# Optimization experiments

Hardware: AMD Instinct MI355X
Metric: run time of the kernel (lower is better)

Reference implementation:

```python
import jax, jax.numpy as jnp
import numpy as np

ROPE_BASE = 10000.0

def _rope_cos_sin(T, d, dtype):
    inv_freq = 1.0 / (ROPE_BASE ** (jnp.arange(0, d, 2, dtype=jnp.float32) / d))
    t = jnp.arange(T, dtype=jnp.float32)
    freqs = t[:, None] * inv_freq[None, :]           # [T, d/2]
    emb = jnp.concatenate([freqs, freqs], axis=-1)   # [T, d]
    return jnp.cos(emb).astype(dtype), jnp.sin(emb).astype(dtype)

def _rotate_half(x):
    x1, x2 = jnp.split(x, 2, axis=-1)
    return jnp.concatenate([-x2, x1], axis=-1)

def setup_inputs() -> dict:
    key = jax.random.key(0)
    k1, k2, k3, k4 = jax.random.split(key, 4)
    B, T, C, H = 4, 4096, 1024, 64
    x = jax.random.normal(k1, (B, T, C), dtype=jnp.float32)
    s = 1.0 / np.sqrt(C)
    Wq = jax.random.normal(k2, (H, C), dtype=jnp.float32) * s
    Wk = jax.random.normal(k3, (H, C), dtype=jnp.float32) * s
    Wv = jax.random.normal(k4, (H, C), dtype=jnp.float32) * s
    return {"x": x, "Wq": Wq, "Wk": Wk, "Wv": Wv}

def reference(x, Wq, Wk, Wv):
    B, T, C = x.shape
    H = Wq.shape[0]
    q = jnp.einsum('btc,hc->bth', x, Wq)
    k = jnp.einsum('btc,hc->bth', x, Wk)
    v = jnp.einsum('btc,hc->bth', x, Wv)
    cos, sin = _rope_cos_sin(T, H, x.dtype)
    q = q * cos + _rotate_half(q) * sin
    k = k * cos + _rotate_half(k) * sin
    # NOTE: original scales by dim_model**-0.5 (C), not head_size
    wei = jnp.einsum('bth,bsh->bts', q, k) * (C ** -0.5)
    causal = jnp.tril(jnp.ones((T, T), dtype=bool))
    wei = jnp.where(causal, wei, -jnp.inf)
    wei = jax.nn.softmax(wei, axis=-1)
    # dropout p=0.0 (identity)
    out = jnp.einsum('bts,bsh->bth', wei, v)
    return out
```

## Files before the change

### kernel.cpp

```cpp
#include <hip/hip_runtime.h>
#include <hip/hip_bf16.h>
#include <math.h>

typedef __attribute__((ext_vector_type(8))) __bf16 bf16x8;
typedef __attribute__((ext_vector_type(4))) float f32x4;
typedef __attribute__((ext_vector_type(16))) float f32x16;
typedef __attribute__((ext_vector_type(4))) float float4_t;
typedef __attribute__((ext_vector_type(4))) unsigned int uint4_t;

#define NB 4
#define TSEQ 4096
#define CD 1024
#define HD 64
#define NCH 16
#define CHT 4

static __device__ __forceinline__ unsigned short f2bf(float f) {
    union { float f; unsigned u; } v; v.f = f;
    unsigned r = v.u + 0x7fffu + ((v.u >> 16) & 1u);
    return (unsigned short)(r >> 16);
}
static __device__ __forceinline__ float bf2f(unsigned short u) {
    union { unsigned int i; float f; } v; v.i = ((unsigned int)u) << 16;
    return v.f;
}
static __device__ __forceinline__ unsigned int pk2(float a, float b) {
    union { __bf16 h[2]; unsigned int u; } x;
    x.h[0] = (__bf16)a; x.h[1] = (__bf16)b;
    return x.u;
}

__global__ __launch_bounds__(256) void wcvt_kernel(const float* __restrict__ wq,
                                                   const float* __restrict__ wk,
                                                   const float* __restrict__ wv,
                                                   unsigned short* __restrict__ wb) {
    int i = blockIdx.x * 256 + threadIdx.x;
    int j = i >> 10;
    int col = i & 1023;
    int jb = j >> 4, off = j & 15;
    int sub = ((jb & 1) << 5) | ((jb & 2) << 3);
    int srcrow = (jb < 8) ? (sub + off) : ((jb - 8) * 16 + off);
    const float* src = (jb < 4) ? wq : ((jb < 8) ? wk : wv);
    wb[i] = f2bf(src[srcrow * 1024 + col]);
}

__global__ __launch_bounds__(256) void qkv_kernel(const float* __restrict__ x,
                                                  const unsigned short* __restrict__ wb,
                                                  unsigned short* __restrict__ qo,
                                                  unsigned short* __restrict__ ko,
                                                  unsigned short* __restrict__ vt) {
    __shared__ unsigned short xs[64][72];
    __shared__ unsigned short ws[64][72];
    const int tid = threadIdx.x;
    const int wave = tid >> 6, lane = tid & 63;
    const int lr = lane & 15;
    const int lk = (lane >> 4) << 3;
    const int rowg = (lane >> 4) << 2;
    const int row0 = blockIdx.x * 64;
    const int cbi = blockIdx.y;
    const int cb = cbi * 64;

    f32x4 acc[4];
#pragma unroll
    for (int i = 0; i < 4; ++i) acc[i] = (f32x4){0.f, 0.f, 0.f, 0.f};

    const int sr = tid >> 2;
    const int sc = (tid & 3) << 4;

    for (int k0 = 0; k0 < CD; k0 += 64) {
        __syncthreads();
        {
            const float4_t* s4 =
                reinterpret_cast<const float4_t*>(x + (size_t)(row0 + sr) * CD + k0 + sc);
            alignas(16) unsigned short tmp[16];
#pragma unroll
            for (int j = 0; j < 4; ++j) {
                float4_t f = s4[j];
#pragma unroll
                for (int e = 0; e < 4; ++e) tmp[j * 4 + e] = f2bf(f[e]);
            }
            *reinterpret_cast<uint4_t*>(&xs[sr][sc]) = *reinterpret_cast<const uint4_t*>(&tmp[0]);
            *reinterpret_cast<uint4_t*>(&xs[sr][sc + 8]) = *reinterpret_cast<const uint4_t*>(&tmp[8]);
        }
        {
            const uint4_t* wsrc =
                reinterpret_cast<const uint4_t*>(wb + (size_t)(cb + sr) * CD + k0 + sc);
            *reinterpret_cast<uint4_t*>(&ws[sr][sc]) = wsrc[0];
            *reinterpret_cast<uint4_t*>(&ws[sr][sc + 8]) = wsrc[1];
        }
        __syncthreads();
#pragma unroll
        for (int kk = 0; kk < 2; ++kk) {
            bf16x8 a = *reinterpret_cast<const bf16x8*>(&xs[wave * 16 + lr][kk * 32 + lk]);
#pragma unroll
            for (int c = 0; c < 4; ++c) {
                bf16x8 bfr = *reinterpret_cast<const bf16x8*>(&ws[c * 16 + lr][kk * 32 + lk]);
                acc[c] = __builtin_amdgcn_mfma_f32_16x16x32_bf16(a, bfr, acc[c], 0, 0, 0);
            }
        }
    }

    const int gr0 = row0 + wave * 16 + rowg;
    const int bidx = gr0 >> 12;
    const int tb = gr0 & (TSEQ - 1);
    if (cbi < 2) {
        unsigned short* o = (cbi == 0) ? qo : ko;
        const float sc2 = (cbi == 0) ? 0.045084218764560315f : 1.0f;
        const float l2b = 0.4152410118609215f;
        const float invf0 = exp2f(-(float)lr * l2b);
        const float invf1 = exp2f(-(float)(lr + 16) * l2b);
#pragma unroll
        for (int r = 0; r < 4; ++r) {
            float t = (float)(tb + r);
            float s0, c0, s1, c1;
            sincosf(t * invf0, &s0, &c0);
            sincosf(t * invf1, &s1, &c1);
            size_t ro = (size_t)(gr0 + r) * HD;
            float lo, hi;
            lo = acc[0][r]; hi = acc[1][r];
            o[ro + 0 + lr]  = f2bf((lo * c0 - hi * s0) * sc2);
            o[ro + 32 + lr] = f2bf((hi * c0 + lo * s0) * sc2);
            lo = acc[2][r]; hi = acc[3][r];
            o[ro + 16 + lr] = f2bf((lo * c1 - hi * s1) * sc2);
            o[ro + 48 + lr] = f2bf((hi * c1 + lo * s1) * sc2);
        }
    } else {
#pragma unroll
        for (int r = 0; r < 4; ++r) {
            size_t vbase = (size_t)bidx * HD * TSEQ + (size_t)(tb + r);
            vt[vbase + (size_t)(0 + lr) * TSEQ]  = f2bf(acc[0][r]);
            vt[vbase + (size_t)(16 + lr) * TSEQ] = f2bf(acc[1][r]);
            vt[vbase + (size_t)(32 + lr) * TSEQ] = f2bf(acc[2][r]);
            vt[vbase + (size_t)(48 + lr) * TSEQ] = f2bf(acc[3][r]);
        }
    }
}

__global__ __launch_bounds__(128, 3) void attn_partial(const unsigned short* __restrict__ q,
                                                       const unsigned short* __restrict__ k,
                                                       const unsigned short* __restrict__ vt,
                                                       unsigned short* __restrict__ po,
                                                       float* __restrict__ pm,
                                                       float* __restrict__ pl) {
    const int chunk = blockIdx.x, qt = blockIdx.y, b = blockIdx.z;
    const int kt0 = chunk * CHT;
    if (kt0 > qt) return;
    const int ktend = min(qt, kt0 + CHT - 1);

    __shared__ unsigned short ks[64][72];
    __shared__ unsigned short vs[64][72];
    const int tid = threadIdx.x;
    const int wave = tid >> 6, lane = tid & 63;
    const int l31 = lane & 31;
    const int h = lane >> 5;
    const int h8 = h << 3;
    const int qrow0 = qt * 64 + wave * 32;
    const int qpos = qrow0 + l31;

    const unsigned short* qb_ = q + ((size_t)(b * TSEQ + qpos)) * HD + h8;
    bf16x8 qf[4];
#pragma unroll
    for (int s = 0; s < 4; ++s)
        qf[s] = *reinterpret_cast<const bf16x8*>(qb_ + 16 * s);

    f32x16 oacc[2];
#pragma unroll
    for (int dt = 0; dt < 2; ++dt)
#pragma unroll
        for (int r = 0; r < 16; ++r) oacc[dt][r] = 0.f;
    float mreg = -INFINITY;
    float lsum = 0.f;

    const int srow = tid >> 1;
    const int scol = (tid & 1) << 5;
    const unsigned short* kbase = k + (size_t)b * TSEQ * HD;
    const unsigned short* vbase = vt + (size_t)b * HD * TSEQ;
    uint4_t kr[4], vr[4];
    {
        const int s0l = kt0 * 64;
        const unsigned short* kp = kbase + (size_t)(s0l + srow) * HD + scol;
        const unsigned short* vp = vbase + (size_t)srow * TSEQ + s0l + scol;
#pragma unroll
        for (int j = 0; j < 4; ++j) {
            kr[j] = *reinterpret_cast<const uint4_t*>(kp + 8 * j);
            vr[j] = *reinterpret_cast<const uint4_t*>(vp + 8 * j);
        }
    }

    for (int kt = kt0; kt <= ktend; ++kt) {
        const int s0 = kt * 64;
        __syncthreads();
#pragma unroll
        for (int j = 0; j < 4; ++j) {
            *reinterpret_cast<uint4_t*>(&ks[srow][scol + 8 * j]) = kr[j];
            *reinterpret_cast<uint4_t*>(&vs[srow][scol + 8 * j]) = vr[j];
        }
        __syncthreads();
        if (kt < ktend) {
            const int s0l = s0 + 64;
            const unsigned short* kp = kbase + (size_t)(s0l + srow) * HD + scol;
            const unsigned short* vp = vbase + (size_t)srow * TSEQ + s0l + scol;
#pragma unroll
            for (int j = 0; j < 4; ++j) {
                kr[j] = *reinterpret_cast<const uint4_t*>(kp + 8 * j);
                vr[j] = *reinterpret_cast<const uint4_t*>(vp + 8 * j);
            }
        }

        f32x16 sacc[2];
#pragma unroll
        for (int blk = 0; blk < 2; ++blk)
#pragma unroll
            for (int r = 0; r < 16; ++r) sacc[blk][r] = 0.f;
        __builtin_amdgcn_s_setprio(1);
#pragma unroll
        for (int s = 0; s < 4; ++s) {
            bf16x8 ka = *reinterpret_cast<const bf16x8*>(&ks[l31][16 * s + h8]);
            bf16x8 kb2 = *reinterpret_cast<const bf16x8*>(&ks[32 + l31][16 * s + h8]);
            sacc[0] = __builtin_amdgcn_mfma_f32_32x32x16_bf16(ka, qf[s], sacc[0], 0, 0, 0);
            sacc[1] = __builtin_amdgcn_mfma_f32_32x32x16_bf16(kb2, qf[s], sacc[1], 0, 0, 0);
        }
        __builtin_amdgcn_s_setprio(0);

        if (kt == qt) {
#pragma unroll
            for (int blk = 0; blk < 2; ++blk)
#pragma unroll
                for (int r = 0; r < 16; ++r) {
                    int kvpos = s0 + 32 * blk + (r & 3) + ((r >> 2) << 3) + (h << 2);
                    if (kvpos > qpos) sacc[blk][r] = -INFINITY;
                }
        }

        float tm[8];
#pragma unroll
        for (int r = 0; r < 8; ++r)
            tm[r] = fmaxf(fmaxf(sacc[0][r], sacc[0][r + 8]),
                          fmaxf(sacc[1][r], sacc[1][r + 8]));
#pragma unroll
        for (int r = 0; r < 4; ++r) tm[r] = fmaxf(tm[r], tm[r + 4]);
        float mx = fmaxf(fmaxf(tm[0], tm[1]), fmaxf(tm[2], tm[3]));
        mx = fmaxf(mx, __shfl_xor(mx, 32, 64));

        const bool newmax = !__all(mx <= mreg + 7.0f);
        if (newmax) {
            float mnew = fmaxf(mreg, mx);
            float corr = __builtin_amdgcn_exp2f(mreg - mnew);
            mreg = mnew;
            lsum *= corr;
#pragma unroll
            for (int dt = 0; dt < 2; ++dt)
#pragma unroll
                for (int r = 0; r < 16; ++r) oacc[dt][r] *= corr;
        }

        float pvv[2][16];
#pragma unroll
        for (int blk = 0; blk < 2; ++blk)
#pragma unroll
            for (int r = 0; r < 16; ++r)
                pvv[blk][r] = __builtin_amdgcn_exp2f(sacc[blk][r] - mreg);
        float ts[8];
#pragma unroll
        for (int r = 0; r < 8; ++r)
            ts[r] = (pvv[0][r] + pvv[0][r + 8]) + (pvv[1][r] + pvv[1][r + 8]);
#pragma unroll
        for (int r = 0; r < 4; ++r) ts[r] += ts[r + 4];
        float psum = (ts[0] + ts[1]) + (ts[2] + ts[3]);
        psum += __shfl_xor(psum, 32, 64);
        lsum += psum;

        unsigned int cw[2][4][2];
#pragma unroll
        for (int blk = 0; blk < 2; ++blk)
#pragma unroll
            for (int G = 0; G < 4; ++G) {
                cw[blk][G][0] = pk2(pvv[blk][4 * G], pvv[blk][4 * G + 1]);
                cw[blk][G][1] = pk2(pvv[blk][4 * G + 2], pvv[blk][4 * G + 3]);
            }

        const bool hif = (h == 1);
        __builtin_amdgcn_s_setprio(1);
#pragma unroll
        for (int s = 0; s < 4; ++s) {
            const int blk = s >> 1, base = (s & 1) << 1;
            unsigned int a0 = cw[blk][base][0],     a1 = cw[blk][base][1];
            unsigned int b0 = cw[blk][base + 1][0], b1 = cw[blk][base + 1][1];
            unsigned int s0w = hif ? a0 : b0;
            unsigned int s1w = hif ? a1 : b1;
            unsigned int r0 = __shfl_xor(s0w, 32, 64);
            unsigned int r1 = __shfl_xor(s1w, 32, 64);
            uint4_t pw;
            pw[0] = hif ? r0 : a0;
            pw[1] = hif ? r1 : a1;
            pw[2] = hif ? b0 : r0;
            pw[3] = hif ? b1 : r1;
            bf16x8 pfrag = *reinterpret_cast<const bf16x8*>(&pw);
            bf16x8 v0 = *reinterpret_cast<const bf16x8*>(&vs[l31][16 * s + h8]);
            bf16x8 v1 = *reinterpret_cast<const bf16x8*>(&vs[32 + l31][16 * s + h8]);
            oacc[0] = __builtin_amdgcn_mfma_f32_32x32x16_bf16(v0, pfrag, oacc[0], 0, 0, 0);
            oacc[1] = __builtin_amdgcn_mfma_f32_32x32x16_bf16(v1, pfrag, oacc[1], 0, 0, 0);
        }
        __builtin_amdgcn_s_setprio(0);
    }

    const int slot = (((b << 6) + qt) << 4) + chunk;
    unsigned short* pob = po + (size_t)slot * 4096;
#pragma unroll
    for (int dt = 0; dt < 2; ++dt)
#pragma unroll
        for (int r = 0; r < 16; ++r) {
            int d = 32 * dt + (r & 3) + ((r >> 2) << 3) + (h << 2);
            pob[d * 64 + wave * 32 + l31] = f2bf(oacc[dt][r]);
        }
    if (h == 0) {
        pm[slot * 64 + wave * 32 + l31] = mreg;
        pl[slot * 64 + wave * 32 + l31] = lsum;
    }
}

__global__ __launch_bounds__(256) void attn_combine(const unsigned short* __restrict__ po,
                                                    const float* __restrict__ pm,
                                                    const float* __restrict__ pl,
                                                    float* __restrict__ out) {
    __shared__ float sm[64][68];
    const int bq = blockIdx.x;
    const int qt = bq & 63;
    const int nch = (qt >> 2) + 1;
    const int qi = threadIdx.x & 63;
    const int dg = threadIdx.x >> 6;
    const int sbase = bq << 4;

    float M = -INFINITY;
    for (int c = 0; c < nch; ++c) M = fmaxf(M, pm[(sbase + c) * 64 + qi]);
    float L = 0.f;
    float acc[16];
#pragma unroll
    for (int j = 0; j < 16; ++j) acc[j] = 0.f;
    for (int c = 0; c < nch; ++c) {
        int s = sbase + c;
        float w = exp2f(pm[s * 64 + qi] - M);
        L += w * pl[s * 64 + qi];
        const unsigned short* p = po + (size_t)s * 4096 + qi;
#pragma unroll
        for (int j = 0; j < 16; ++j) acc[j] += w * bf2f(p[(dg * 16 + j) * 64]);
    }
    float inv = 1.f / L;
#pragma unroll
    for (int j = 0; j < 16; ++j) sm[qi][dg * 16 + j] = acc[j] * inv;
    __syncthreads();
    const int row = threadIdx.x >> 2;
    const int cg = (threadIdx.x & 3) << 4;
    float4_t* dst = reinterpret_cast<float4_t*>(out + (size_t)bq * 4096 + row * 64 + cg);
#pragma unroll
    for (int v4 = 0; v4 < 4; ++v4) {
        float4_t f;
#pragma unroll
        for (int e = 0; e < 4; ++e) f[e] = sm[row][cg + v4 * 4 + e];
        dst[v4] = f;
    }
}

extern "C" void kernel_launch(void* const* d_in, const int* in_sizes, int n_in,
                              void* d_out, int out_size, void* d_ws, size_t ws_size,
                              hipStream_t stream) {
    const float* x = (const float*)d_in[0];
    const float* wq = (const float*)d_in[1];
    const float* wk = (const float*)d_in[2];
    const float* wv = (const float*)d_in[3];
    float* out = (float*)d_out;

    unsigned short* wb = (unsigned short*)d_ws;
    unsigned short* qb = wb + 3 * HD * CD;
    unsigned short* kb = qb + (size_t)NB * TSEQ * HD;
    unsigned short* vtb = kb + (size_t)NB * TSEQ * HD;
    unsigned short* pob = vtb + (size_t)NB * TSEQ * HD;
    float* pm = (float*)(pob + (size_t)4096 * 4096);
    float* pl = pm + (size_t)4096 * 64;

    wcvt_kernel<<<768, 256, 0, stream>>>(wq, wk, wv, wb);
    qkv_kernel<<<dim3(256, 3), 256, 0, stream>>>(x, wb, qb, kb, vtb);
    attn_partial<<<dim3(NCH, 64, NB), 128, 0, stream>>>(qb, kb, vtb, pob, pm, pl);
    attn_combine<<<NB * 64, 256, 0, stream>>>(pob, pm, pl, out);
}
```

Before: 74.02 us.

## Halve split-K chunk size, reverse query-tile order, parallelize combine over head dims

The key-tile chunk size drops from 4 to 2, doubling the number of split-K chunks to 32. This gives more, shorter partial-attention blocks for better load balance across CUs. Query tiles are launched in reverse order so the heaviest tiles start first. The combine kernel is split across 4 blocks per query tile along the head dimension, and its chunk maxima are loaded into registers and reduced as a tree. In exchange, the partial output and its global-memory traffic double, and the combine work grows.

New measurement: 76.44 us. 3.3% more time.

```diff
diff --git a/kernel.cpp b/kernel.cpp
--- a/kernel.cpp
+++ b/kernel.cpp
@@ -12,8 +12,8 @@
 #define TSEQ 4096
 #define CD 1024
 #define HD 64
-#define NCH 16
-#define CHT 4
+#define NCH 32
+#define CHT 2
 
 static __device__ __forceinline__ unsigned short f2bf(float f) {
     union { float f; unsigned u; } v; v.f = f;
@@ -142,7 +142,8 @@
                                                        unsigned short* __restrict__ po,
                                                        float* __restrict__ pm,
                                                        float* __restrict__ pl) {
-    const int chunk = blockIdx.x, qt = blockIdx.y, b = blockIdx.z;
+    const int chunk = blockIdx.x, b = blockIdx.z;
+    const int qt = 63 - blockIdx.y;
     const int kt0 = chunk * CHT;
     if (kt0 > qt) return;
     const int ktend = min(qt, kt0 + CHT - 1);
@@ -304,7 +305,7 @@
         __builtin_amdgcn_s_setprio(0);
     }
 
-    const int slot = (((b << 6) + qt) << 4) + chunk;
+    const int slot = (((b << 6) + qt) << 5) + chunk;
     unsigned short* pob = po + (size_t)slot * 4096;
 #pragma unroll
     for (int dt = 0; dt < 2; ++dt)
@@ -323,42 +324,54 @@
                                                     const float* __restrict__ pm,
                                                     const float* __restrict__ pl,
                                                     float* __restrict__ out) {
-    __shared__ float sm[64][68];
+    __shared__ float sm[64][17];
     const int bq = blockIdx.x;
+    const int dg = blockIdx.y;
     const int qt = bq & 63;
-    const int nch = (qt >> 2) + 1;
+    const int nch = (qt >> 1) + 1;
     const int qi = threadIdx.x & 63;
-    const int dg = threadIdx.x >> 6;
-    const int sbase = bq << 4;
-
-    float M = -INFINITY;
-    for (int c = 0; c < nch; ++c) M = fmaxf(M, pm[(sbase + c) * 64 + qi]);
+    const int jj = threadIdx.x >> 6;
+    const int sbase = bq << 5;
+
+    float pmv[NCH];
+#pragma unroll
+    for (int c = 0; c < NCH; ++c)
+        pmv[c] = (c < nch) ? pm[(size_t)(sbase + c) * 64 + qi] : -INFINITY;
+    float tmv[NCH];
+#pragma unroll
+    for (int c = 0; c < NCH; ++c) tmv[c] = pmv[c];
+#pragma unroll
+    for (int s = NCH / 2; s >= 1; s >>= 1)
+#pragma unroll
+        for (int c = 0; c < NCH / 2; ++c)
+            if (c < s) tmv[c] = fmaxf(tmv[c], tmv[c + s]);
+    const float M = tmv[0];
+
     float L = 0.f;
-    float acc[16];
-#pragma unroll
-    for (int j = 0; j < 16; ++j) acc[j] = 0.f;
+    float a0 = 0.f, a1 = 0.f, a2 = 0.f, a3 = 0.f;
+    const int dbase = dg * 16 + jj * 4;
+#pragma unroll 4
     for (int c = 0; c < nch; ++c) {
-        int s = sbase + c;
-        float w = exp2f(pm[s * 64 + qi] - M);
-        L += w * pl[s * 64 + qi];
-        const unsigned short* p = po + (size_t)s * 4096 + qi;
-#pragma unroll
-        for (int j = 0; j < 16; ++j) acc[j] += w * bf2f(p[(dg * 16 + j) * 64]);
-    }
-    float inv = 1.f / L;
-#pragma unroll
-    for (int j = 0; j < 16; ++j) sm[qi][dg * 16 + j] = acc[j] * inv;
+        float w = exp2f(pmv[c] - M);
+        L += w * pl[(size_t)(sbase + c) * 64 + qi];
+        const unsigned short* p = po + (size_t)(sbase + c) * 4096 + dbase * 64 + qi;
+        a0 += w * bf2f(p[0]);
+        a1 += w * bf2f(p[64]);
+        a2 += w * bf2f(p[128]);
+        a3 += w * bf2f(p[192]);
+    }
+    const float inv = 1.f / L;
+    sm[qi][jj * 4 + 0] = a0 * inv;
+    sm[qi][jj * 4 + 1] = a1 * inv;
+    sm[qi][jj * 4 + 2] = a2 * inv;
+    sm[qi][jj * 4 + 3] = a3 * inv;
     __syncthreads();
     const int row = threadIdx.x >> 2;
-    const int cg = (threadIdx.x & 3) << 4;
-    float4_t* dst = reinterpret_cast<float4_t*>(out + (size_t)bq * 4096 + row * 64 + cg);
-#pragma unroll
-    for (int v4 = 0; v4 < 4; ++v4) {
-        float4_t f;
-#pragma unroll
-        for (int e = 0; e < 4; ++e) f[e] = sm[row][cg + v4 * 4 + e];
-        dst[v4] = f;
-    }
+    const int c4 = (threadIdx.x & 3) << 2;
+    float4_t f;
+#pragma unroll
+    for (int e = 0; e < 4; ++e) f[e] = sm[row][c4 + e];
+    *reinterpret_cast<float4_t*>(out + (size_t)bq * 4096 + row * 64 + dg * 16 + c4) = f;
 }
 
 extern "C" void kernel_launch(void* const* d_in, const int* in_sizes, int n_in,
@@ -375,11 +388,11 @@
     unsigned short* kb = qb + (size_t)NB * TSEQ * HD;
     unsigned short* vtb = kb + (size_t)NB * TSEQ * HD;
     unsigned short* pob = vtb + (size_t)NB * TSEQ * HD;
-    float* pm = (float*)(pob + (size_t)4096 * 4096);
-    float* pl = pm + (size_t)4096 * 64;
+    float* pm = (float*)(pob + (size_t)8192 * 4096);
+    float* pl = pm + (size_t)8192 * 64;
 
     wcvt_kernel<<<768, 256, 0, stream>>>(wq, wk, wv, wb);
     qkv_kernel<<<dim3(256, 3), 256, 0, stream>>>(x, wb, qb, kb, vtb);
     attn_partial<<<dim3(NCH, 64, NB), 128, 0, stream>>>(qb, kb, vtb, pob, pm, pl);
-    attn_combine<<<NB * 64, 256, 0, stream>>>(pob, pm, pl, out);
-}
+    attn_combine<<<dim3(NB * 64, 4), 256, 0, stream>>>(pob, pm, pl, out);
+}
```
